# Performance work log

Measured on AMD Instinct MI355X. Metric: run time of the kernel, lower is better.

The kernel has to match this reference:

```python
import jax, jax.numpy as jnp
import numpy as np

HEAD_SIZE = 64

def setup_inputs() -> dict:
    key = jax.random.key(0)
    ks = jax.random.split(key, 6)
    B, T, C = 4, 4096, 1024
    H = HEAD_SIZE
    return {
        "q": jax.random.normal(ks[0], (B, T, C), dtype=jnp.float32),
        "k": jax.random.normal(ks[1], (B, T, C), dtype=jnp.float32),
        "v": jax.random.normal(ks[2], (B, T, C), dtype=jnp.float32),
        "Wq": jax.random.normal(ks[3], (H, C), dtype=jnp.float32) * (C ** -0.5),
        "Wk": jax.random.normal(ks[4], (H, C), dtype=jnp.float32) * (C ** -0.5),
        "Wv": jax.random.normal(ks[5], (H, C), dtype=jnp.float32) * (C ** -0.5),
    }

def reference(q, k, v, Wq, Wk, Wv):
    # dropout p=0.0 -> identity (module applies F.dropout before each projection)
    T = q.shape[1]
    scale = HEAD_SIZE ** -0.5
    Q = jnp.einsum('btc,hc->bth', q, Wq)   # [B,T,H]
    K = jnp.einsum('btc,hc->bth', k, Wk)   # [B,T,H]
    V = jnp.einsum('btc,hc->bth', v, Wv)   # [B,T,H]
    scores = jnp.einsum('bth,bsh->bts', Q, K) * scale  # [B,T,T]
    # non-standard mask: tril with diagonal=1 (each query sees positions <= i+1)
    mask = jnp.tril(jnp.ones((T, T), dtype=bool), k=1)
    scores = jnp.where(mask, scores, -jnp.inf)
    # double scaling as in the original: softmax(scores * head_size**-0.5)
    weights = jax.nn.softmax(scores * scale, axis=-1)
    return jnp.einsum('bts,bsh->bth', weights, V)
```

## Files before the change

kernel.cpp:

```cpp
#include <hip/hip_runtime.h>
#include <hip/hip_bf16.h>

#define BB 4
#define TT 4096
#define CC 1024
#define HH 64

typedef _Float16 f16;
typedef __attribute__((ext_vector_type(8))) _Float16 f16x8;
typedef __attribute__((ext_vector_type(4))) _Float16 f16x4;
typedef __attribute__((ext_vector_type(4))) float f32x4;

#define MFMA32(a,b,c) __builtin_amdgcn_mfma_f32_16x16x32_f16((a),(b),(c),0,0,0)
#define MFMA16(a,b,c) __builtin_amdgcn_mfma_f32_16x16x16f16((a),(b),(c),0,0,0)

#define WF_ELEMS (3 * 32 * 4 * 64 * 8)
#define CHUNK_F16 1024
#define PB_F16 (256 * CHUNK_F16)

static __device__ __forceinline__ void gl_lds16(const void* g, void* l) {
  __builtin_amdgcn_global_load_lds(
      (const __attribute__((address_space(1))) unsigned int*)g,
      (__attribute__((address_space(3))) unsigned int*)l, 16, 0, 0);
}

static __device__ __forceinline__ f16x8 pack2(f32x4 a, f32x4 b) {
  f16x8 r;
  r[0]=(f16)a[0]; r[1]=(f16)a[1]; r[2]=(f16)a[2]; r[3]=(f16)a[3];
  r[4]=(f16)b[0]; r[5]=(f16)b[1]; r[6]=(f16)b[2]; r[7]=(f16)b[3];
  return r;
}

__global__ __launch_bounds__(64) void wrepack_kernel(
    const float* __restrict__ Wqg, const float* __restrict__ Wkg,
    const float* __restrict__ Wvg, f16* __restrict__ Wf)
{
  const int bx = blockIdx.x;
  const int nt = bx & 3;
  const int kc = (bx >> 2) & 31;
  const int p  = bx >> 7;
  const float* W = (p == 0) ? Wqg : (p == 1) ? Wkg : Wvg;
  const float sc = (p == 0) ? (1.4426950408889634f / 64.0f) : 1.0f;

  const int lane = threadIdx.x;
  const int l16 = lane & 15, quad = lane >> 4;
  const float* src = W + (size_t)(nt * 16 + l16) * CC + kc * 32 + quad * 8;
  f32x4 a = *(const f32x4*)src;
  f32x4 b = *(const f32x4*)(src + 4);
  f16x8 r;
  #pragma unroll
  for (int j = 0; j < 4; ++j) { r[j] = (f16)(a[j] * sc); r[j + 4] = (f16)(b[j] * sc); }
  *(f16x8*)(Wf + (size_t)bx * 512 + lane * 8) = r;
}

__global__ __launch_bounds__(256, 3) void proj_kernel(
    const float* __restrict__ qg, const float* __restrict__ kg, const float* __restrict__ vg,
    const f16* __restrict__ Wf,
    f16* __restrict__ Qf, f16* __restrict__ Kf, f16* __restrict__ Vf)
{
  __shared__ float Xs[2][64][64];

  const float* X; f16* O; const int p = blockIdx.y;
  if (p == 0)      { X = qg; O = Qf; }
  else if (p == 1) { X = kg; O = Kf; }
  else             { X = vg; O = Vf; }

  const int tid  = threadIdx.x;
  const int w    = tid >> 6;
  const int lane = tid & 63;
  const int quad = lane >> 4;
  const int l16  = lane & 15;
  const int r0   = blockIdx.x * 64;

  const float* Xld[4];
  int wr[4], ws[4];
  #pragma unroll
  for (int s = 0; s < 4; ++s) {
    const int R = w * 16 + s * 4 + (lane >> 4);
    Xld[s] = X + (size_t)(r0 + R) * CC + (lane & 15) * 4;
    wr[s] = R;
    ws[s] = ((lane & 15) ^ ((R & 7) << 1)) * 4;
  }
  const f16* wbase = Wf + (size_t)p * 128 * 512 + lane * 8;

  f32x4 acc[4];
  #pragma unroll
  for (int nt = 0; nt < 4; ++nt) acc[nt] = (f32x4){0.f, 0.f, 0.f, 0.f};

  const int sw = (l16 & 7) << 1;

  f32x4 La[4], Lb[4];
  #pragma unroll
  for (int s = 0; s < 4; ++s) La[s] = *(const f32x4*)(Xld[s]);

#define PROJ_PHASE(IT, BUF, CUR, NXT)                                         \
  {                                                                           \
    const int itn = ((IT) < 15) ? (IT) + 1 : 15;                              \
    _Pragma("unroll")                                                         \
    for (int s = 0; s < 4; ++s)                                               \
      NXT[s] = *(const f32x4*)(Xld[s] + itn * 64);                            \
    __builtin_amdgcn_sched_barrier(0);                                        \
    _Pragma("unroll")                                                         \
    for (int s = 0; s < 4; ++s)                                               \
      *(f32x4*)&Xs[BUF][wr[s]][ws[s]] = CUR[s];                               \
    __builtin_amdgcn_sched_barrier(0);                                        \
    _Pragma("unroll")                                                         \
    for (int kk = 0; kk < 2; ++kk) {                                          \
      const int c0 = kk * 8 + quad * 2;                                       \
      f32x4 a0 = *(const f32x4*)&Xs[BUF][w * 16 + l16][(c0 ^ sw) * 4];        \
      f32x4 a1 = *(const f32x4*)&Xs[BUF][w * 16 + l16][((c0 + 1) ^ sw) * 4];  \
      f16x8 af = pack2(a0, a1);                                               \
      _Pragma("unroll")                                                       \
      for (int nt = 0; nt < 4; ++nt) {                                        \
        f16x8 bf = *(const f16x8*)(wbase + (size_t)(((IT) * 2 + kk) * 4 + nt) * 512); \
        acc[nt] = MFMA32(af, bf, acc[nt]);                                    \
      }                                                                       \
    }                                                                         \
  }

  #pragma unroll
  for (int ih = 0; ih < 8; ++ih) {
    PROJ_PHASE(2 * ih,     0, La, Lb)
    PROJ_PHASE(2 * ih + 1, 1, Lb, La)
  }
#undef PROJ_PHASE

  f16 (*Ls)[66] = (f16(*)[66])&Xs[0][w * 16][0];
  #pragma unroll
  for (int nt = 0; nt < 4; ++nt)
    #pragma unroll
    for (int r = 0; r < 4; ++r)
      Ls[quad * 4 + r][nt * 16 + l16] = (f16)acc[nt][r];
  const size_t chunk = (size_t)blockIdx.x * 4 + w;
  if (p < 2) {
    #pragma unroll
    for (int h = 0; h < 2; ++h) {
      f16x8 t = *(const f16x8*)&Ls[l16][h * 32 + quad * 8];
      *(f16x8*)(O + (chunk * 2 + h) * 512 + lane * 8) = t;
    }
  } else {
    #pragma unroll
    for (int np = 0; np < 2; ++np) {
      f16x8 t;
      #pragma unroll
      for (int j = 0; j < 8; ++j)
        t[j] = Ls[quad * 4 + (j & 3)][(2 * np + (j >> 2)) * 16 + l16];
      *(f16x8*)(O + (chunk * 2 + np) * 512 + lane * 8) = t;
    }
  }
}

__device__ __forceinline__ void attn_tile(
    int b, int j, int a, int e, int wave, int quad, int l16, int lane, int sp,
    const f16* __restrict__ Qf, const f16* __restrict__ Kf, const f16* __restrict__ Vf,
    f16 (*Ks)[8][64][8], f16 (*Vs)[8][64][8],
    float* __restrict__ Opart, float* __restrict__ lpart)
{
  const int m0 = j * 64 + wave * 16;

  const f16* Kfb = Kf + (size_t)b * PB_F16;
  const f16* Vfb = Vf + (size_t)b * PB_F16;
  const f16* Qfb = Qf + (size_t)b * PB_F16;

  f16x8 qa0 = *(const f16x8*)(Qfb + ((size_t)(m0 >> 4) * 2 + 0) * 512 + lane * 8);
  f16x8 qa1 = *(const f16x8*)(Qfb + ((size_t)(m0 >> 4) * 2 + 1) * 512 + lane * 8);

  f32x4 o[4];
  float lsum = 0.f;
  #pragma unroll
  for (int nt = 0; nt < 4; ++nt) o[nt] = (f32x4){0.f, 0.f, 0.f, 0.f};

  __syncthreads();

  if (a < e) {
    #pragma unroll
    for (int jj = 0; jj < 2; ++jj) {
      const int idx = 2 * wave + jj;
      gl_lds16(Kfb + (size_t)a * 4096 + idx * 512 + lane * 8, &Ks[0][idx][0][0]);
      gl_lds16(Vfb + (size_t)a * 4096 + idx * 512 + lane * 8, &Vs[0][idx][0][0]);
    }
  }

  for (int st = a; st < e; ++st) {
    const int buf = (st - a) & 1;
    __syncthreads();
    if (st + 1 < e) {
      #pragma unroll
      for (int jj = 0; jj < 2; ++jj) {
        const int idx = 2 * wave + jj;
        gl_lds16(Kfb + (size_t)(st + 1) * 4096 + idx * 512 + lane * 8, &Ks[buf ^ 1][idx][0][0]);
        gl_lds16(Vfb + (size_t)(st + 1) * 4096 + idx * 512 + lane * 8, &Vs[buf ^ 1][idx][0][0]);
      }
    }
    const int s0 = st * 64;

    f32x4 sc[4];
    #pragma unroll
    for (int ct = 0; ct < 4; ++ct) {
      f16x8 k0 = *(const f16x8*)&Ks[buf][ct * 2][lane][0];
      f16x8 k1 = *(const f16x8*)&Ks[buf][ct * 2 + 1][lane][0];
      f32x4 z = (f32x4){0.f, 0.f, 0.f, 0.f};
      z = MFMA32(k0, qa0, z);
      sc[ct] = MFMA32(k1, qa1, z);
    }

    const bool domask = (s0 + 63) > (m0 + 1);
    f16x4 pa[4];
    #pragma unroll
    for (int ct = 0; ct < 4; ++ct) {
      #pragma unroll
      for (int r = 0; r < 4; ++r) {
        float x = sc[ct][r];
        if (domask) {
          const int key = s0 + ct * 16 + quad * 4 + r;
          if (key > m0 + l16 + 1) x = -__builtin_inff();
        }
        const float pv = __builtin_amdgcn_exp2f(x);
        lsum += pv;
        pa[ct][r] = (f16)pv;
      }
    }

    #pragma unroll
    for (int ct = 0; ct < 4; ++ct) {
      #pragma unroll
      for (int np = 0; np < 2; ++np) {
        f16x8 vv = *(const f16x8*)&Vs[buf][ct * 2 + np][lane][0];
        f16x4 blo = __builtin_shufflevector(vv, vv, 0, 1, 2, 3);
        f16x4 bhi = __builtin_shufflevector(vv, vv, 4, 5, 6, 7);
        o[2 * np]     = MFMA16(pa[ct], blo, o[2 * np]);
        o[2 * np + 1] = MFMA16(pa[ct], bhi, o[2 * np + 1]);
      }
    }
  }

  lsum += __shfl_xor(lsum, 16, 64);
  lsum += __shfl_xor(lsum, 32, 64);
  const size_t rbase = (size_t)(sp * BB + b) * TT;
  if (quad == 0) lpart[rbase + m0 + l16] = lsum;
  #pragma unroll
  for (int nt = 0; nt < 4; ++nt)
    #pragma unroll
    for (int r = 0; r < 4; ++r)
      Opart[(rbase + m0 + quad * 4 + r) * HH + nt * 16 + l16] = o[nt][r];
}

__global__ __launch_bounds__(256) void attn_kernel(
    const f16* __restrict__ Qf, const f16* __restrict__ Kf, const f16* __restrict__ Vf,
    float* __restrict__ Opart, float* __restrict__ lpart, int S)
{
  __shared__ f16 Ks[2][8][64][8];
  __shared__ f16 Vs[2][8][64][8];

  const int pr = blockIdx.x;
  const int sp = blockIdx.y;
  const int b  = blockIdx.z;
  const int tid  = threadIdx.x;
  const int wave = tid >> 6;
  const int lane = tid & 63;
  const int quad = lane >> 4;
  const int l16  = lane & 15;

  const int j1 = pr, j2 = 63 - pr;
  const int n1 = min(j1 + 2, 64), n2 = min(j2 + 2, 64);
  const int tot = n1 + n2;
  const int lo = tot * sp / S, hi = tot * (sp + 1) / S;
  const int a1 = min(lo, n1), e1 = min(hi, n1);
  const int a2 = max(lo - n1, 0), e2 = max(hi - n1, 0);

  attn_tile(b, j1, a1, e1, wave, quad, l16, lane, sp, Qf, Kf, Vf, Ks, Vs, Opart, lpart);
  attn_tile(b, j2, a2, e2, wave, quad, l16, lane, sp, Qf, Kf, Vf, Ks, Vs, Opart, lpart);
}

__global__ __launch_bounds__(256) void combine_kernel(
    const float* __restrict__ Opart, const float* __restrict__ lpart,
    float* __restrict__ out, int S)
{
  const int idx = blockIdx.x * 256 + threadIdx.x;
  const int row = idx >> 4;
  const int c   = (idx & 15) * 4;
  float l = 0.f;
  f32x4 s = (f32x4){0.f, 0.f, 0.f, 0.f};
  for (int p = 0; p < S; ++p) {
    l += lpart[(size_t)p * BB * TT + row];
    s += *(const f32x4*)&Opart[((size_t)p * BB * TT + row) * HH + c];
  }
  const float inv = 1.0f / l;
  *(f32x4*)&out[(size_t)row * HH + c] = s * inv;
}

extern "C" void kernel_launch(void* const* d_in, const int* in_sizes, int n_in,
                              void* d_out, int out_size, void* d_ws, size_t ws_size,
                              hipStream_t stream)
{
  const float* q  = (const float*)d_in[0];
  const float* k  = (const float*)d_in[1];
  const float* v  = (const float*)d_in[2];
  const float* Wq = (const float*)d_in[3];
  const float* Wk = (const float*)d_in[4];
  const float* Wv = (const float*)d_in[5];
  float* out = (float*)d_out;

  const size_t n = (size_t)BB * TT * HH;
  const size_t need8 = (WF_ELEMS + 3 * n) * sizeof(f16)
                     + 8 * n * sizeof(float) + 8 * (size_t)BB * TT * sizeof(float);
  const int S = (ws_size >= need8) ? 8 : 4;

  f16* Wf = (f16*)d_ws;
  f16* Qf = Wf + WF_ELEMS;
  f16* Kf = Qf + n;
  f16* Vf = Kf + n;
  float* Opart = (float*)(Vf + n);
  float* lpart = Opart + (size_t)S * n;

  wrepack_kernel<<<dim3(384), 64, 0, stream>>>(Wq, Wk, Wv, Wf);
  proj_kernel<<<dim3(256, 3), 256, 0, stream>>>(q, k, v, Wf, Qf, Kf, Vf);
  attn_kernel<<<dim3(32, S, BB), 256, 0, stream>>>(Qf, Kf, Vf, Opart, lpart, S);
  combine_kernel<<<dim3(1024), 256, 0, stream>>>(Opart, lpart, out, S);
}
```

Measured before the change: 234.6 us.

## Load K/V tiles directly from global into registers, dropping LDS staging

Replaces the double-buffered global_load_lds staging of K and V tiles in shared memory with per-wave direct global loads into registers. All block-level barriers go away, and launch bounds now request 4 blocks per CU. The cost is that each of the 4 waves re-reads the same K/V tile from global/L2, quadrupling that traffic. Loads are no longer prefetched a step ahead, so more latency may be exposed unless occupancy hides it.

```diff
diff --git a/kernel.cpp b/kernel.cpp
--- a/kernel.cpp
+++ b/kernel.cpp
@@ -153,7 +153,6 @@
 __device__ __forceinline__ void attn_tile(
     int b, int j, int a, int e, int wave, int quad, int l16, int lane, int sp,
     const f16* __restrict__ Qf, const f16* __restrict__ Kf, const f16* __restrict__ Vf,
-    f16 (*Ks)[8][64][8], f16 (*Vs)[8][64][8],
     float* __restrict__ Opart, float* __restrict__ lpart)
 {
   const int m0 = j * 64 + wave * 16;
@@ -170,39 +169,26 @@
   #pragma unroll
   for (int nt = 0; nt < 4; ++nt) o[nt] = (f32x4){0.f, 0.f, 0.f, 0.f};
 
-  __syncthreads();
-
-  if (a < e) {
-    #pragma unroll
-    for (int jj = 0; jj < 2; ++jj) {
-      const int idx = 2 * wave + jj;
-      gl_lds16(Kfb + (size_t)a * 4096 + idx * 512 + lane * 8, &Ks[0][idx][0][0]);
-      gl_lds16(Vfb + (size_t)a * 4096 + idx * 512 + lane * 8, &Vs[0][idx][0][0]);
-    }
-  }
-
   for (int st = a; st < e; ++st) {
-    const int buf = (st - a) & 1;
-    __syncthreads();
-    if (st + 1 < e) {
-      #pragma unroll
-      for (int jj = 0; jj < 2; ++jj) {
-        const int idx = 2 * wave + jj;
-        gl_lds16(Kfb + (size_t)(st + 1) * 4096 + idx * 512 + lane * 8, &Ks[buf ^ 1][idx][0][0]);
-        gl_lds16(Vfb + (size_t)(st + 1) * 4096 + idx * 512 + lane * 8, &Vs[buf ^ 1][idx][0][0]);
-      }
-    }
     const int s0 = st * 64;
+    const f16* kb = Kfb + (size_t)st * 4096 + lane * 8;
+    const f16* vb = Vfb + (size_t)st * 4096 + lane * 8;
+
+    f16x8 kf[8];
+    #pragma unroll
+    for (int i = 0; i < 8; ++i) kf[i] = *(const f16x8*)(kb + (size_t)i * 512);
 
     f32x4 sc[4];
     #pragma unroll
     for (int ct = 0; ct < 4; ++ct) {
-      f16x8 k0 = *(const f16x8*)&Ks[buf][ct * 2][lane][0];
-      f16x8 k1 = *(const f16x8*)&Ks[buf][ct * 2 + 1][lane][0];
       f32x4 z = (f32x4){0.f, 0.f, 0.f, 0.f};
-      z = MFMA32(k0, qa0, z);
-      sc[ct] = MFMA32(k1, qa1, z);
-    }
+      z = MFMA32(kf[ct * 2], qa0, z);
+      sc[ct] = MFMA32(kf[ct * 2 + 1], qa1, z);
+    }
+
+    f16x8 vf[8];
+    #pragma unroll
+    for (int i = 0; i < 8; ++i) vf[i] = *(const f16x8*)(vb + (size_t)i * 512);
 
     const bool domask = (s0 + 63) > (m0 + 1);
     f16x4 pa[4];
@@ -225,7 +211,7 @@
     for (int ct = 0; ct < 4; ++ct) {
       #pragma unroll
       for (int np = 0; np < 2; ++np) {
-        f16x8 vv = *(const f16x8*)&Vs[buf][ct * 2 + np][lane][0];
+        f16x8 vv = vf[ct * 2 + np];
         f16x4 blo = __builtin_shufflevector(vv, vv, 0, 1, 2, 3);
         f16x4 bhi = __builtin_shufflevector(vv, vv, 4, 5, 6, 7);
         o[2 * np]     = MFMA16(pa[ct], blo, o[2 * np]);
@@ -245,13 +231,10 @@
       Opart[(rbase + m0 + quad * 4 + r) * HH + nt * 16 + l16] = o[nt][r];
 }
 
-__global__ __launch_bounds__(256) void attn_kernel(
+__global__ __launch_bounds__(256, 4) void attn_kernel(
     const f16* __restrict__ Qf, const f16* __restrict__ Kf, const f16* __restrict__ Vf,
     float* __restrict__ Opart, float* __restrict__ lpart, int S)
 {
-  __shared__ f16 Ks[2][8][64][8];
-  __shared__ f16 Vs[2][8][64][8];
-
   const int pr = blockIdx.x;
   const int sp = blockIdx.y;
   const int b  = blockIdx.z;
@@ -268,8 +251,8 @@
   const int a1 = min(lo, n1), e1 = min(hi, n1);
   const int a2 = max(lo - n1, 0), e2 = max(hi - n1, 0);
 
-  attn_tile(b, j1, a1, e1, wave, quad, l16, lane, sp, Qf, Kf, Vf, Ks, Vs, Opart, lpart);
-  attn_tile(b, j2, a2, e2, wave, quad, l16, lane, sp, Qf, Kf, Vf, Ks, Vs, Opart, lpart);
+  attn_tile(b, j1, a1, e1, wave, quad, l16, lane, sp, Qf, Kf, Vf, Opart, lpart);
+  attn_tile(b, j2, a2, e2, wave, quad, l16, lane, sp, Qf, Kf, Vf, Opart, lpart);
 }
 
 __global__ __launch_bounds__(256) void combine_kernel(
```

Measured after the change: 240.8 us. 1.03x slower.
